# Optimization experiments

Measured on AMD Instinct MI355X. Metric: run time of the kernel, lower is better.

Reference implementation:

```python
import jax, jax.numpy as jnp
import numpy as np

N_NODES = 100000
N_EDGES = 1600000
IN_CH = 32
HID = 128
EDGE_DIM = 16
BN_EPS = 1e-5


def setup_inputs() -> dict:
    key = jax.random.key(0)
    ks = jax.random.split(key, 32)
    f32 = jnp.float32

    def w(k, shape, scale):
        return jax.random.normal(k, shape, dtype=f32) * scale

    inp = {
        'x': w(ks[0], (N_NODES, IN_CH), 1.0),
        'edge_index': jax.random.randint(ks[1], (2, N_EDGES), 0, N_NODES, dtype=jnp.int32),
        'edge_attr': w(ks[2], (N_EDGES, EDGE_DIM), 1.0),
        # layer 0: in=32 -> out=128
        'l0_We': w(ks[3], (EDGE_DIM, IN_CH), 0.1),
        'l0_be': jnp.zeros((IN_CH,), f32),
        'l0_W1': w(ks[4], (IN_CH, HID), 0.1),
        'l0_b1': jnp.zeros((HID,), f32),
        'l0_W2': w(ks[5], (HID, HID), 0.1),
        'l0_b2': jnp.zeros((HID,), f32),
        'l0_gamma': jnp.ones((HID,), f32),
        'l0_beta': jnp.zeros((HID,), f32),
        # layer 1: 128 -> 128
        'l1_We': w(ks[6], (EDGE_DIM, HID), 0.1),
        'l1_be': jnp.zeros((HID,), f32),
        'l1_W1': w(ks[7], (HID, HID), 0.1),
        'l1_b1': jnp.zeros((HID,), f32),
        'l1_W2': w(ks[8], (HID, HID), 0.1),
        'l1_b2': jnp.zeros((HID,), f32),
        'l1_gamma': jnp.ones((HID,), f32),
        'l1_beta': jnp.zeros((HID,), f32),
        # head MLP: hidden -> hidden -> 1
        'head_W1': w(ks[9], (HID, HID), 0.1),
        'head_b1': jnp.zeros((HID,), f32),
        'head_W2': w(ks[10], (HID, 1), 0.1),
        'head_b2': jnp.zeros((1,), f32),
    }
    return inp


def _gnblock(x, src, dst, e, We, be, W1, b1, W2, b2, gamma, beta):
    # GINE-style message passing: gather -> edge message -> scatter-sum
    msg = jax.nn.relu(x[src] + e @ We + be)              # [E, d_in]
    agg = jax.ops.segment_sum(msg, dst, num_segments=N_NODES)  # [N, d_in]
    h = x + agg                                          # GIN combine (eps=0)
    h = jax.nn.relu(h @ W1 + b1) @ W2 + b2               # 2-layer MLP
    # batch norm over the node dimension (use_norm=True)
    mu = jnp.mean(h, axis=0)
    var = jnp.var(h, axis=0)
    h = (h - mu) * jax.lax.rsqrt(var + BN_EPS) * gamma + beta
    return jax.nn.relu(h)


def reference(x, edge_index, edge_attr,
              l0_We, l0_be, l0_W1, l0_b1, l0_W2, l0_b2, l0_gamma, l0_beta,
              l1_We, l1_be, l1_W1, l1_b1, l1_W2, l1_b2, l1_gamma, l1_beta,
              head_W1, head_b1, head_W2, head_b2):
    src, dst = edge_index[0], edge_index[1]
    h = _gnblock(x, src, dst, edge_attr,
                 l0_We, l0_be, l0_W1, l0_b1, l0_W2, l0_b2, l0_gamma, l0_beta)
    h = _gnblock(h, src, dst, edge_attr,
                 l1_We, l1_be, l1_W1, l1_b1, l1_W2, l1_b2, l1_gamma, l1_beta)
    # MLPBlock head + sigmoid -> per-node selection probability [N, 1]
    out = jax.nn.relu(h @ head_W1 + head_b1) @ head_W2 + head_b2
    return jax.nn.sigmoid(out)
```

## Files before the change

kernel.cpp:

```cpp
#include <hip/hip_runtime.h>

#define NN 100000
#define NE 1600000
#define TMAX 193760
#define NRANGES 24220

typedef unsigned int uint32;
typedef unsigned long long ull;
typedef __attribute__((ext_vector_type(8))) short bf16x8;
typedef __attribute__((ext_vector_type(4))) float f32x4;

__device__ __forceinline__ unsigned short f2bf(float f) {
  unsigned int u = __float_as_uint(f);
  unsigned int r = (u + 0x7fffu + ((u >> 16) & 1u)) >> 16;
  return (unsigned short)r;
}
__device__ __forceinline__ float bf2f(unsigned short u) {
  return __uint_as_float(((unsigned int)u) << 16);
}
__device__ __forceinline__ unsigned int pack2(float a, float b) {
  return (unsigned int)f2bf(a) | ((unsigned int)f2bf(b) << 16);
}
__device__ __forceinline__ uint32 pack2ru(float a, float b) {
  const uint32 ua = __float_as_uint(a) + 0x8000u;
  const uint32 ub = __float_as_uint(b) + 0x8000u;
  return (ua >> 16) | (ub & 0xffff0000u);
}
__device__ __forceinline__ float row16_sum(float x) {
  x += __int_as_float(__builtin_amdgcn_mov_dpp(__float_as_int(x), 0x128, 0xf, 0xf, false));
  x += __int_as_float(__builtin_amdgcn_mov_dpp(__float_as_int(x), 0x124, 0xf, 0xf, false));
  x += __int_as_float(__builtin_amdgcn_mov_dpp(__float_as_int(x), 0x122, 0xf, 0xf, false));
  x += __int_as_float(__builtin_amdgcn_mov_dpp(__float_as_int(x), 0x121, 0xf, 0xf, false));
  return x;
}

__device__ __forceinline__ void wconv_body(const float* __restrict__ src,
    unsigned short* __restrict__ dst, int K, int N, int b)
{
  const int i = b * 256 + threadIdx.x;
  if (i < K * N) {
    const int n = i / K, k = i - n * K;
    dst[i] = f2bf(src[k * N + n]);
  }
}

__global__ __launch_bounds__(256) void conv_all(
    const float* __restrict__ l0W1, const float* __restrict__ l0W2,
    const float* __restrict__ l1W1, const float* __restrict__ l1W2,
    const float* __restrict__ hW1,  const float* __restrict__ l0We,
    const float* __restrict__ l1We, const float* __restrict__ x,
    unsigned short* __restrict__ W1t0, unsigned short* __restrict__ W2t0,
    unsigned short* __restrict__ W1t1, unsigned short* __restrict__ W2t1,
    unsigned short* __restrict__ hW1t, unsigned short* __restrict__ Wet0,
    unsigned short* __restrict__ Wet1, unsigned short* __restrict__ xb)
{
  int b = blockIdx.x;
  if (b < 16)  { wconv_body(l0W1, W1t0, 32, 128, b); return; }  b -= 16;
  if (b < 64)  { wconv_body(l0W2, W2t0, 128, 128, b); return; } b -= 64;
  if (b < 64)  { wconv_body(l1W1, W1t1, 128, 128, b); return; } b -= 64;
  if (b < 64)  { wconv_body(l1W2, W2t1, 128, 128, b); return; } b -= 64;
  if (b < 64)  { wconv_body(hW1,  hW1t, 128, 128, b); return; } b -= 64;
  if (b < 2)   { wconv_body(l0We, Wet0, 16, 32, b); return; }   b -= 2;
  if (b < 8)   { wconv_body(l1We, Wet1, 16, 128, b); return; }  b -= 8;
  const int i = b * 256 + threadIdx.x;
  if (i * 8 < NN * 32) {
    const float4 a = ((const float4*)x)[i * 2];
    const float4 d = ((const float4*)x)[i * 2 + 1];
    uint4 o;
    o.x = pack2(a.x, a.y); o.y = pack2(a.z, a.w);
    o.z = pack2(d.x, d.y); o.w = pack2(d.z, d.w);
    ((uint4*)xb)[i] = o;
  }
}

__global__ __launch_bounds__(256) void hist_kernel(
    const int* __restrict__ ei, uint32* __restrict__ deg)
{
  const int e = blockIdx.x * 256 + threadIdx.x;
  if (e < NE) atomicAdd(&deg[ei[NE + e]], 1u);
}

__global__ __launch_bounds__(256) void offsets2_kernel(
    const uint32* __restrict__ deg, uint32* __restrict__ toff,
    uint32* __restrict__ eoff, ull* __restrict__ counter)
{
  __shared__ ull s[256];
  __shared__ ull base;
  const int tid = threadIdx.x;
  const int n = blockIdx.x * 256 + tid;
  const uint32 d = (n < NN) ? deg[n] : 0u;
  const uint32 tc = (d + 15u) >> 4;
  const ull v = ((ull)tc << 32) | (ull)d;
  s[tid] = v;
  __syncthreads();
#pragma unroll
  for (int st = 1; st < 256; st <<= 1) {
    ull w = (tid >= st) ? s[tid - st] : 0ull;
    __syncthreads();
    s[tid] += w;
    __syncthreads();
  }
  if (tid == 255) base = atomicAdd(counter, s[255]);
  __syncthreads();
  if (n < NN) {
    const ull t = base + (s[tid] - v);
    toff[n] = (uint32)(t >> 32);
    eoff[n] = (uint32)t;
  }
}

__global__ __launch_bounds__(256) void snode_fill(
    const uint32* __restrict__ toff, const uint32* __restrict__ deg,
    int* __restrict__ snode)
{
  const int n = blockIdx.x * 256 + threadIdx.x;
  if (n < NN) {
    const uint32 t0 = toff[n];
    const uint32 tc = (deg[n] + 15u) >> 4;
    for (uint32 i = 0; i < tc; ++i) snode[t0 + i] = n;
  }
}

__global__ __launch_bounds__(256) void fill_kernel(
    const int* __restrict__ ei, const uint32* __restrict__ eoff,
    uint32* __restrict__ cnt, uint2* __restrict__ esrc2)
{
  const int e = blockIdx.x * 256 + threadIdx.x;
  if (e < NE) {
    const int dst = ei[NE + e];
    const uint32 pos = eoff[dst] + atomicAdd(&cnt[dst], 1u);
    esrc2[pos] = make_uint2((uint32)e, (uint32)ei[e]);
  }
}

template<int D, int NCT, bool GEA>
__global__ __launch_bounds__(256) void flat_agg5(
    const int* __restrict__ snode, const uint32* __restrict__ toff,
    const uint32* __restrict__ eoff, const uint32* __restrict__ deg,
    const uint2* __restrict__ esrc2, const float* __restrict__ ea,
    unsigned short* __restrict__ eabc,
    const unsigned short* __restrict__ hsrc,
    const unsigned short* __restrict__ Wet, const float* __restrict__ be,
    const ull* __restrict__ tot, float* __restrict__ agg)
{
  const int tid = threadIdx.x;
  const int wid = tid >> 6;
  const int lane = tid & 63;
  const int c = lane & 15;
  const int g = lane >> 4;
  constexpr bool HALF = (NCT * 16 != D);
  int range, ch0;
  if (HALF) { range = blockIdx.x * 2 + (wid >> 1); ch0 = (wid & 1) * (NCT * 16); }
  else      { range = blockIdx.x * 4 + wid;        ch0 = 0; }
  const int tile0 = range * 8;
  const uint32 ntile = (uint32)((*tot) >> 32);
  if ((uint32)tile0 >= ntile) return;

  bf16x8 wf[NCT];
#pragma unroll
  for (int ct = 0; ct < NCT; ++ct) {
    const int chA = ch0 + (c >> 2) * (NCT * 4) + ct * 4 + (c & 3);
    uint4 u = make_uint4(0u, 0u, 0u, 0u);
    if (g < 2) u = *(const uint4*)&Wet[chA * 16 + g * 8];
    else if (g == 2) u.x = (0xFE96u << 16) | (uint32)f2bf(be[chA]);
    union { uint4 u4; bf16x8 v; } cv; cv.u4 = u;
    wf[ct] = cv.v;
  }

  int sn8 = -1, pk8 = 0, p_ = 0;
  if (lane < 8) {
    sn8 = snode[tile0 + lane];
    if (sn8 >= 0) {
      const uint32 to = toff[sn8], dg = deg[sn8], eo = eoff[sn8];
      const int k = tile0 + lane - (int)to;
      p_ = (int)eo + k * 16;
      int rv = (int)dg - k * 16; if (rv > 16) rv = 16;
      const int fl = (k == 0 ? 1 : 0) |
                     ((k == (int)((dg + 15u) >> 4) - 1) ? 2 : 0);
      pk8 = (rv << 7) | (fl << 12);
    }
  }
  const int p0base = __shfl(p_, 0);
  if (lane < 8 && sn8 >= 0) pk8 |= (p_ - p0base);

  const uint2 q0 = esrc2[(size_t)p0base + lane];
  const uint2 q1 = esrc2[(size_t)p0base + 64 + lane];

  float acc[NCT][4];
#pragma unroll
  for (int ct = 0; ct < NCT; ++ct) {
    acc[ct][0] = 0.f; acc[ct][1] = 0.f; acc[ct][2] = 0.f; acc[ct][3] = 0.f;
  }
  int openNode = -1; bool openFull = false, openClosed = false;

  auto flushOpen = [&](bool storeOK) {
#pragma unroll
    for (int ct = 0; ct < NCT; ++ct)
#pragma unroll
      for (int j = 0; j < 4; ++j)
        acc[ct][j] = row16_sum(acc[ct][j]);
    float4 sv = make_float4(0.f, 0.f, 0.f, 0.f);
#pragma unroll
    for (int ct = 0; ct < NCT; ++ct)
      if (c == ct)
        sv = make_float4(acc[ct][0], acc[ct][1], acc[ct][2], acc[ct][3]);
    if (c < NCT) {
      float* p = &agg[(size_t)openNode * D + ch0 + g * (NCT * 4) + c * 4];
      if (storeOK) {
        *(float4*)p = sv;
      } else {
        atomicAdd(p + 0, sv.x); atomicAdd(p + 1, sv.y);
        atomicAdd(p + 2, sv.z); atomicAdd(p + 3, sv.w);
      }
    }
  };

  auto issue = [&](int t, float4& E0, float4& E1, uint4& afu,
                   uint4& h0, uint4& h1, int& n_, int& mt_) {
    n_ = __shfl(sn8, t);
    mt_ = __shfl(pk8, t);
    const int d0 = mt_ & 127;
    const int rem = (mt_ >> 7) & 31;
    const int idx = d0 + ((c < rem) ? c : 0);
    const int li = idx & 63;
    const uint32 sA = (uint32)__shfl((int)q0.y, li);
    const uint32 sB = (uint32)__shfl((int)q1.y, li);
    const int src = (int)((idx & 64) ? sB : sA);
    if constexpr (GEA) {
      const uint32 eA = (uint32)__shfl((int)q0.x, li);
      const uint32 eB = (uint32)__shfl((int)q1.x, li);
      const int e = (int)((idx & 64) ? eB : eA);
      if (g < 2) {
        E0 = *(const float4*)&ea[(size_t)e * 16 + g * 8];
        E1 = *(const float4*)&ea[(size_t)e * 16 + g * 8 + 4];
      }
    } else {
      if (g < 2) afu = *(const uint4*)&eabc[((size_t)p0base + idx) * 16 + g * 8];
    }
    h0 = *(const uint4*)&hsrc[(size_t)src * D + ch0 + g * (NCT * 4)];
    if constexpr (NCT == 4)
      h1 = *(const uint4*)&hsrc[(size_t)src * D + ch0 + g * (NCT * 4) + 8];
  };

  auto compute = [&](const float4 E0, const float4 E1, uint4 afu,
                     const uint4 h0, const uint4 h1, const int n, const int mt) {
    if (n < 0) return;
    const int rem = (mt >> 7) & 31;
    const int fl = mt >> 12;
    if (n != openNode) {
      if (openNode >= 0) {
        flushOpen(openFull);
#pragma unroll
        for (int ct = 0; ct < NCT; ++ct) {
          acc[ct][0] = 0.f; acc[ct][1] = 0.f;
          acc[ct][2] = 0.f; acc[ct][3] = 0.f;
        }
      }
      openNode = n; openFull = (fl & 1) != 0; openClosed = false;
    }
    if (fl & 2) openClosed = true;
    if constexpr (GEA) {
      afu.x = pack2ru(E0.x, E0.y); afu.y = pack2ru(E0.z, E0.w);
      afu.z = pack2ru(E1.x, E1.y); afu.w = pack2ru(E1.z, E1.w);
      if (g < 2) {
        const int d0 = mt & 127;
        const int idx = d0 + ((c < rem) ? c : 0);
        *(uint4*)&eabc[((size_t)p0base + idx) * 16 + g * 8] = afu;
      }
    }
    bf16x8 afv;
    {
      uint4 u = make_uint4(0u, 0u, 0u, 0u);
      if (g < 2) u = afu;
      else if (g == 2) u.x = (c < rem) ? 0x3f80u : 0x3f803f80u;
      union { uint4 u4; bf16x8 v; } cv; cv.u4 = u; afv = cv.v;
    }
#pragma unroll
    for (int ct = 0; ct < NCT; ++ct) {
      f32x4 pre = __builtin_amdgcn_mfma_f32_16x16x32_bf16(
          wf[ct], afv, (f32x4){0.f, 0.f, 0.f, 0.f}, 0, 0, 0);
      uint32 w0, w1;
      if constexpr (NCT == 4) {
        const uint4 hu = (ct < 2) ? h0 : h1;
        w0 = (ct & 1) ? hu.z : hu.x;
        w1 = (ct & 1) ? hu.w : hu.y;
      } else {
        w0 = (ct & 1) ? h0.z : h0.x;
        w1 = (ct & 1) ? h0.w : h0.y;
      }
      acc[ct][0] += fmaxf(pre[0] + bf2f((unsigned short)(w0 & 0xffffu)), 0.f);
      acc[ct][1] += fmaxf(pre[1] + bf2f((unsigned short)(w0 >> 16)), 0.f);
      acc[ct][2] += fmaxf(pre[2] + bf2f((unsigned short)(w1 & 0xffffu)), 0.f);
      acc[ct][3] += fmaxf(pre[3] + bf2f((unsigned short)(w1 >> 16)), 0.f);
    }
  };

  float4 eA0, eA1, eB0, eB1, eC0, eC1;
  uint4 aA = make_uint4(0,0,0,0), aB = make_uint4(0,0,0,0), aC = make_uint4(0,0,0,0);
  uint4 h0A = make_uint4(0,0,0,0), h1A = make_uint4(0,0,0,0);
  uint4 h0B = make_uint4(0,0,0,0), h1B = make_uint4(0,0,0,0);
  uint4 h0C = make_uint4(0,0,0,0), h1C = make_uint4(0,0,0,0);
  int nA = -1, mA = 0, nB = -1, mB = 0, nC = -1, mC = 0;

  issue(0, eA0, eA1, aA, h0A, h1A, nA, mA);
  issue(1, eB0, eB1, aB, h0B, h1B, nB, mB);
  issue(2, eC0, eC1, aC, h0C, h1C, nC, mC);
  compute(eA0, eA1, aA, h0A, h1A, nA, mA); issue(3, eA0, eA1, aA, h0A, h1A, nA, mA);
  compute(eB0, eB1, aB, h0B, h1B, nB, mB); issue(4, eB0, eB1, aB, h0B, h1B, nB, mB);
  compute(eC0, eC1, aC, h0C, h1C, nC, mC); issue(5, eC0, eC1, aC, h0C, h1C, nC, mC);
  compute(eA0, eA1, aA, h0A, h1A, nA, mA); issue(6, eA0, eA1, aA, h0A, h1A, nA, mA);
  compute(eB0, eB1, aB, h0B, h1B, nB, mB); issue(7, eB0, eB1, aB, h0B, h1B, nB, mB);
  compute(eC0, eC1, aC, h0C, h1C, nC, mC);
  compute(eA0, eA1, aA, h0A, h1A, nA, mA);
  compute(eB0, eB1, aB, h0B, h1B, nB, mB);
  if (openNode >= 0) flushOpen(openFull && openClosed);
}

template<int DIN, bool ABF16>
__global__ __launch_bounds__(256) void mlp_mfma(
    const float* __restrict__ a32, const unsigned short* __restrict__ abf,
    const float* __restrict__ agg,
    const unsigned short* __restrict__ W1t, const float* __restrict__ b1,
    const unsigned short* __restrict__ W2t, const float* __restrict__ b2,
    float* __restrict__ outp, float* __restrict__ stats, int nChunks)
{
  constexpr int P1 = (DIN == 128) ? 136 : 40;
  constexpr int KS1 = DIN / 32;
  __shared__ __align__(16) unsigned short hin[64 * P1];
  __shared__ __align__(16) unsigned short tls[64 * 136];
  const int tid = threadIdx.x;
  const int w = tid >> 6;
  const int lane = tid & 63;
  const int c = lane & 15, g = lane >> 4;
  const int cw = w * 32;

  bf16x8 B1[2][KS1], B2[2][4];
#pragma unroll
  for (int ct = 0; ct < 2; ++ct)
#pragma unroll
    for (int kk = 0; kk < KS1; ++kk)
      B1[ct][kk] = *(const bf16x8*)&W1t[(cw + ct * 16 + c) * DIN + kk * 32 + g * 8];
#pragma unroll
  for (int ct = 0; ct < 2; ++ct)
#pragma unroll
    for (int kk = 0; kk < 4; ++kk)
      B2[ct][kk] = *(const bf16x8*)&W2t[(cw + ct * 16 + c) * 128 + kk * 32 + g * 8];
  const float b1c0 = b1[cw + c], b1c1 = b1[cw + 16 + c];
  const float b2c0 = b2[cw + c], b2c1 = b2[cw + 16 + c];
  float lsum0 = 0.f, lsum1 = 0.f, lsq0 = 0.f, lsq1 = 0.f;

  for (int chunk = blockIdx.x; chunk < nChunks; chunk += gridDim.x) {
    const int base = chunk * 64;
    if constexpr (DIN == 128) {
#pragma unroll
      for (int p = 0; p < 4; ++p) {
        const int idx = tid + 256 * p;
        const int n = idx >> 4, k8 = idx & 15;
        const int node = base + n;
        uint4 ov = make_uint4(0u, 0u, 0u, 0u);
        if (node < NN) {
          const float4 g0 = *(const float4*)&agg[node * 128 + k8 * 8];
          const float4 g1 = *(const float4*)&agg[node * 128 + k8 * 8 + 4];
          const uint4 hv = *(const uint4*)&abf[node * 128 + k8 * 8];
          ov.x = pack2(bf2f((unsigned short)(hv.x & 0xffffu)) + g0.x,
                       bf2f((unsigned short)(hv.x >> 16)) + g0.y);
          ov.y = pack2(bf2f((unsigned short)(hv.y & 0xffffu)) + g0.z,
                       bf2f((unsigned short)(hv.y >> 16)) + g0.w);
          ov.z = pack2(bf2f((unsigned short)(hv.z & 0xffffu)) + g1.x,
                       bf2f((unsigned short)(hv.z >> 16)) + g1.y);
          ov.w = pack2(bf2f((unsigned short)(hv.w & 0xffffu)) + g1.z,
                       bf2f((unsigned short)(hv.w >> 16)) + g1.w);
        }
        *(uint4*)&hin[n * P1 + k8 * 8] = ov;
      }
    } else {
      const int n = tid >> 2, k8 = tid & 3;
      const int node = base + n;
      uint4 ov = make_uint4(0u, 0u, 0u, 0u);
      if (node < NN) {
        const float4 x0 = *(const float4*)&a32[node * 32 + k8 * 8];
        const float4 x1 = *(const float4*)&a32[node * 32 + k8 * 8 + 4];
        const float4 g0 = *(const float4*)&agg[node * 32 + k8 * 8];
        const float4 g1 = *(const float4*)&agg[node * 32 + k8 * 8 + 4];
        ov.x = pack2(x0.x + g0.x, x0.y + g0.y);
        ov.y = pack2(x0.z + g0.z, x0.w + g0.w);
        ov.z = pack2(x1.x + g1.x, x1.y + g1.y);
        ov.w = pack2(x1.z + g1.z, x1.w + g1.w);
      }
      *(uint4*)&hin[n * P1 + k8 * 8] = ov;
    }
    __syncthreads();
#pragma unroll
    for (int nt = 0; nt < 4; ++nt) {
      bf16x8 af[KS1];
#pragma unroll
      for (int kk = 0; kk < KS1; ++kk)
        af[kk] = *(const bf16x8*)&hin[(nt * 16 + c) * P1 + kk * 32 + g * 8];
      f32x4 acc0 = {0.f, 0.f, 0.f, 0.f}, acc1 = {0.f, 0.f, 0.f, 0.f};
#pragma unroll
      for (int kk = 0; kk < KS1; ++kk) {
        acc0 = __builtin_amdgcn_mfma_f32_16x16x32_bf16(af[kk], B1[0][kk], acc0, 0, 0, 0);
        acc1 = __builtin_amdgcn_mfma_f32_16x16x32_bf16(af[kk], B1[1][kk], acc1, 0, 0, 0);
      }
#pragma unroll
      for (int j = 0; j < 4; ++j) {
        const int row = nt * 16 + g * 4 + j;
        tls[row * 136 + cw + c]      = f2bf(fmaxf(acc0[j] + b1c0, 0.f));
        tls[row * 136 + cw + 16 + c] = f2bf(fmaxf(acc1[j] + b1c1, 0.f));
      }
    }
    __syncthreads();
#pragma unroll
    for (int nt = 0; nt < 4; ++nt) {
      bf16x8 af[4];
#pragma unroll
      for (int kk = 0; kk < 4; ++kk)
        af[kk] = *(const bf16x8*)&tls[(nt * 16 + c) * 136 + kk * 32 + g * 8];
      f32x4 acc0 = {0.f, 0.f, 0.f, 0.f}, acc1 = {0.f, 0.f, 0.f, 0.f};
#pragma unroll
      for (int kk = 0; kk < 4; ++kk) {
        acc0 = __builtin_amdgcn_mfma_f32_16x16x32_bf16(af[kk], B2[0][kk], acc0, 0, 0, 0);
        acc1 = __builtin_amdgcn_mfma_f32_16x16x32_bf16(af[kk], B2[1][kk], acc1, 0, 0, 0);
      }
#pragma unroll
      for (int j = 0; j < 4; ++j) {
        const int node = base + nt * 16 + g * 4 + j;
        if (node < NN) {
          const float v0 = acc0[j] + b2c0;
          const float v1 = acc1[j] + b2c1;
          outp[node * 128 + cw + c] = v0;
          outp[node * 128 + cw + 16 + c] = v1;
          lsum0 += v0; lsq0 += v0 * v0;
          lsum1 += v1; lsq1 += v1 * v1;
        }
      }
    }
  }
  lsum0 += __shfl_xor(lsum0, 16); lsum0 += __shfl_xor(lsum0, 32);
  lsum1 += __shfl_xor(lsum1, 16); lsum1 += __shfl_xor(lsum1, 32);
  lsq0  += __shfl_xor(lsq0, 16);  lsq0  += __shfl_xor(lsq0, 32);
  lsq1  += __shfl_xor(lsq1, 16);  lsq1  += __shfl_xor(lsq1, 32);
  if (lane < 16) {
    atomicAdd(&stats[cw + lane], lsum0);
    atomicAdd(&stats[cw + 16 + lane], lsum1);
    atomicAdd(&stats[128 + cw + lane], lsq0);
    atomicAdd(&stats[128 + cw + 16 + lane], lsq1);
  }
}

__global__ void bn_finalize(float* __restrict__ stats,
                            const float* __restrict__ gamma,
                            const float* __restrict__ beta)
{
  const int cc = threadIdx.x;
  const float inv_n = 1.0f / (float)NN;
  const float mu = stats[cc] * inv_n;
  float var = stats[128 + cc] * inv_n - mu * mu;
  var = fmaxf(var, 0.f);
  const float rs = rsqrtf(var + 1e-5f);
  const float sc = rs * gamma[cc];
  stats[256 + cc] = sc;
  stats[384 + cc] = beta[cc] - mu * sc;
}

__global__ __launch_bounds__(256) void bn_apply_bf16(
    const float* __restrict__ h, const float* __restrict__ stats,
    unsigned short* __restrict__ hb)
{
  const int idx = blockIdx.x * 256 + threadIdx.x;
  const int c4 = (idx & 31) * 4;
  const float4 sc = *(const float4*)&stats[256 + c4];
  const float4 sh = *(const float4*)&stats[384 + c4];
  const float4 v = ((const float4*)h)[idx];
  const float r0 = fmaxf(fmaf(v.x, sc.x, sh.x), 0.f);
  const float r1 = fmaxf(fmaf(v.y, sc.y, sh.y), 0.f);
  const float r2 = fmaxf(fmaf(v.z, sc.z, sh.z), 0.f);
  const float r3 = fmaxf(fmaf(v.w, sc.w, sh.w), 0.f);
  uint2 o;
  o.x = pack2(r0, r1);
  o.y = pack2(r2, r3);
  ((uint2*)hb)[idx] = o;
}

__global__ __launch_bounds__(256) void head_bn(
    const float* __restrict__ hpre, const float* __restrict__ stats,
    const unsigned short* __restrict__ W1t, const float* __restrict__ b1,
    const float* __restrict__ w2, const float* __restrict__ b2,
    float* __restrict__ out, int nChunks)
{
  __shared__ float pl[4][64];
  const int tid = threadIdx.x;
  const int w = tid >> 6;
  const int lane = tid & 63;
  const int c = lane & 15, g = lane >> 4;
  const int cw = w * 32;

  bf16x8 B1[2][4];
#pragma unroll
  for (int ct = 0; ct < 2; ++ct)
#pragma unroll
    for (int kk = 0; kk < 4; ++kk)
      B1[ct][kk] = *(const bf16x8*)&W1t[(cw + ct * 16 + c) * 128 + kk * 32 + g * 8];
  const float b1c0 = b1[cw + c], b1c1 = b1[cw + 16 + c];
  const float w2c0 = w2[cw + c], w2c1 = w2[cw + 16 + c];
  const float b2v = b2[0];
  float4 scq[4][2], shq[4][2];
#pragma unroll
  for (int kk = 0; kk < 4; ++kk) {
    const int cb = kk * 32 + g * 8;
    scq[kk][0] = *(const float4*)&stats[256 + cb];
    scq[kk][1] = *(const float4*)&stats[256 + cb + 4];
    shq[kk][0] = *(const float4*)&stats[384 + cb];
    shq[kk][1] = *(const float4*)&stats[384 + cb + 4];
  }

  for (int chunk = blockIdx.x; chunk < nChunks; chunk += gridDim.x) {
    const int base = chunk * 64;
    float p[4][4];
#pragma unroll
    for (int nt = 0; nt < 4; ++nt) {
      const int node = base + nt * 16 + c;
      bf16x8 af[4];
#pragma unroll
      for (int kk = 0; kk < 4; ++kk) {
        uint4 u = make_uint4(0u, 0u, 0u, 0u);
        if (node < NN) {
          const float4 v0 = *(const float4*)&hpre[(size_t)node * 128 + kk * 32 + g * 8];
          const float4 v1 = *(const float4*)&hpre[(size_t)node * 128 + kk * 32 + g * 8 + 4];
          const float4 s0 = scq[kk][0], s1 = scq[kk][1];
          const float4 h0 = shq[kk][0], h1 = shq[kk][1];
          u.x = pack2(fmaxf(fmaf(v0.x, s0.x, h0.x), 0.f),
                      fmaxf(fmaf(v0.y, s0.y, h0.y), 0.f));
          u.y = pack2(fmaxf(fmaf(v0.z, s0.z, h0.z), 0.f),
                      fmaxf(fmaf(v0.w, s0.w, h0.w), 0.f));
          u.z = pack2(fmaxf(fmaf(v1.x, s1.x, h1.x), 0.f),
                      fmaxf(fmaf(v1.y, s1.y, h1.y), 0.f));
          u.w = pack2(fmaxf(fmaf(v1.z, s1.z, h1.z), 0.f),
                      fmaxf(fmaf(v1.w, s1.w, h1.w), 0.f));
        }
        union { uint4 u4; bf16x8 v; } cv; cv.u4 = u;
        af[kk] = cv.v;
      }
      f32x4 acc0 = {0.f, 0.f, 0.f, 0.f}, acc1 = {0.f, 0.f, 0.f, 0.f};
#pragma unroll
      for (int kk = 0; kk < 4; ++kk) {
        acc0 = __builtin_amdgcn_mfma_f32_16x16x32_bf16(af[kk], B1[0][kk], acc0, 0, 0, 0);
        acc1 = __builtin_amdgcn_mfma_f32_16x16x32_bf16(af[kk], B1[1][kk], acc1, 0, 0, 0);
      }
#pragma unroll
      for (int j = 0; j < 4; ++j)
        p[nt][j] = fmaxf(acc0[j] + b1c0, 0.f) * w2c0 +
                   fmaxf(acc1[j] + b1c1, 0.f) * w2c1;
    }
#pragma unroll
    for (int dd = 1; dd <= 8; dd <<= 1)
#pragma unroll
      for (int nt = 0; nt < 4; ++nt)
#pragma unroll
        for (int j = 0; j < 4; ++j)
          p[nt][j] += __shfl_xor(p[nt][j], dd);
    if (c == 0) {
#pragma unroll
      for (int nt = 0; nt < 4; ++nt)
#pragma unroll
        for (int j = 0; j < 4; ++j)
          pl[w][nt * 16 + g * 4 + j] = p[nt][j];
    }
    __syncthreads();
    if (tid < 64) {
      const int node = base + tid;
      if (node < NN) {
        const float s = pl[0][tid] + pl[1][tid] + pl[2][tid] + pl[3][tid] + b2v;
        out[node] = 1.f / (1.f + expf(-s));
      }
    }
    __syncthreads();
  }
}

extern "C" void kernel_launch(void* const* d_in, const int* in_sizes, int n_in,
                              void* d_out, int out_size, void* d_ws, size_t ws_size,
                              hipStream_t stream)
{
  const float* x    = (const float*)d_in[0];
  const int*   ei   = (const int*)  d_in[1];
  const float* ea   = (const float*)d_in[2];
  const float* l0We = (const float*)d_in[3];
  const float* l0be = (const float*)d_in[4];
  const float* l0W1 = (const float*)d_in[5];
  const float* l0b1 = (const float*)d_in[6];
  const float* l0W2 = (const float*)d_in[7];
  const float* l0b2 = (const float*)d_in[8];
  const float* l0g  = (const float*)d_in[9];
  const float* l0bt = (const float*)d_in[10];
  const float* l1We = (const float*)d_in[11];
  const float* l1be = (const float*)d_in[12];
  const float* l1W1 = (const float*)d_in[13];
  const float* l1b1 = (const float*)d_in[14];
  const float* l1W2 = (const float*)d_in[15];
  const float* l1b2 = (const float*)d_in[16];
  const float* l1g  = (const float*)d_in[17];
  const float* l1bt = (const float*)d_in[18];
  const float* hW1  = (const float*)d_in[19];
  const float* hb1  = (const float*)d_in[20];
  const float* hW2  = (const float*)d_in[21];
  const float* hb2  = (const float*)d_in[22];
  float* out = (float*)d_out;

  float*  A    = (float*)d_ws;
  float*  AGG  = A + (size_t)NN * 128;
  unsigned short* hb = (unsigned short*)(AGG + (size_t)NN * 128);
  unsigned short* xb = hb + (size_t)NN * 128;
  uint32* deg     = (uint32*)(xb + (size_t)NN * 32);
  uint32* cnt     = deg + NN;
  uint32* toff    = cnt + NN;
  uint32* eoff    = toff + NN;
  ull*    counter = (ull*)(eoff + NN);
  int*    snode   = (int*)(counter + 2);
  uint2*  esrc2   = (uint2*)(snode + TMAX);
  float*  st0     = (float*)(esrc2 + NE + 128);
  float*  st1     = st0 + 512;
  unsigned short* W1t0 = (unsigned short*)(st1 + 512);
  unsigned short* W2t0 = W1t0 + 4096;
  unsigned short* W1t1 = W2t0 + 16384;
  unsigned short* W2t1 = W1t1 + 16384;
  unsigned short* hW1t = W2t1 + 16384;
  unsigned short* Wet0 = hW1t + 16384;
  unsigned short* Wet1 = Wet0 + 512;
  unsigned short* eabc = Wet1 + 2048;

  const size_t needed = (size_t)((char*)(eabc + (size_t)NE * 16) - (char*)d_ws);
  if (ws_size < needed) return;

  hipMemsetAsync(deg, 0, (size_t)2 * NN * 4, stream);
  hipMemsetAsync(counter, 0, 16, stream);
  hipMemsetAsync(snode, 0xFF, (size_t)TMAX * 4, stream);
  hipMemsetAsync(st0, 0, 4096, stream);
  hipMemsetAsync(AGG, 0, (size_t)NN * 32 * 4, stream);

  const int nChunks = (NN + 63) / 64;
  const int eBlocks = (NE + 255) / 256;

  conv_all<<<16 + 64 * 4 + 2 + 8 + 1563, 256, 0, stream>>>(
      l0W1, l0W2, l1W1, l1W2, hW1, l0We, l1We, x,
      W1t0, W2t0, W1t1, W2t1, hW1t, Wet0, Wet1, xb);

  hist_kernel<<<eBlocks, 256, 0, stream>>>(ei, deg);
  offsets2_kernel<<<(NN + 255) / 256, 256, 0, stream>>>(deg, toff, eoff, counter);
  snode_fill<<<(NN + 255) / 256, 256, 0, stream>>>(toff, deg, snode);
  fill_kernel<<<eBlocks, 256, 0, stream>>>(ei, eoff, cnt, esrc2);

  flat_agg5<32, 2, true><<<NRANGES / 4, 256, 0, stream>>>(
      snode, toff, eoff, deg, esrc2, ea, eabc, xb, Wet0, l0be, counter, AGG);
  mlp_mfma<32, false><<<782, 256, 0, stream>>>(x, (const unsigned short*)nullptr,
      AGG, W1t0, l0b1, W2t0, l0b2, A, st0, nChunks);
  hipMemsetAsync(AGG, 0, (size_t)NN * 128 * 4, stream);
  bn_finalize<<<1, 128, 0, stream>>>(st0, l0g, l0bt);
  bn_apply_bf16<<<(NN * 32) / 256, 256, 0, stream>>>(A, st0, hb);

  flat_agg5<128, 4, false><<<NRANGES / 2, 256, 0, stream>>>(
      snode, toff, eoff, deg, esrc2, ea, eabc, hb, Wet1, l1be, counter, AGG);
  mlp_mfma<128, true><<<782, 256, 0, stream>>>((const float*)nullptr, hb,
      AGG, W1t1, l1b1, W2t1, l1b2, A, st1, nChunks);
  bn_finalize<<<1, 128, 0, stream>>>(st1, l1g, l1bt);

  head_bn<<<782, 256, 0, stream>>>(A, st1, hW1t, hb1, hW2, hb2, out, nChunks);
}
```

Baseline: 554.0 us.

## Swap MFMA operand roles so channels map to lanes and edges to accumulator rows

After: 541.3 us. 2.3% less time.

```diff
diff --git a/kernel.cpp b/kernel.cpp
--- a/kernel.cpp
+++ b/kernel.cpp
@@ -25,13 +25,6 @@
   const uint32 ua = __float_as_uint(a) + 0x8000u;
   const uint32 ub = __float_as_uint(b) + 0x8000u;
   return (ua >> 16) | (ub & 0xffff0000u);
-}
-__device__ __forceinline__ float row16_sum(float x) {
-  x += __int_as_float(__builtin_amdgcn_mov_dpp(__float_as_int(x), 0x128, 0xf, 0xf, false));
-  x += __int_as_float(__builtin_amdgcn_mov_dpp(__float_as_int(x), 0x124, 0xf, 0xf, false));
-  x += __int_as_float(__builtin_amdgcn_mov_dpp(__float_as_int(x), 0x122, 0xf, 0xf, false));
-  x += __int_as_float(__builtin_amdgcn_mov_dpp(__float_as_int(x), 0x121, 0xf, 0xf, false));
-  return x;
 }
 
 __device__ __forceinline__ void wconv_body(const float* __restrict__ src,
@@ -133,8 +126,8 @@
   }
 }
 
-template<int D, int NCT, bool GEA>
-__global__ __launch_bounds__(256) void flat_agg5(
+template<int D, int NB, bool GEA>
+__global__ __launch_bounds__(256) void flat_agg8(
     const int* __restrict__ snode, const uint32* __restrict__ toff,
     const uint32* __restrict__ eoff, const uint32* __restrict__ deg,
     const uint2* __restrict__ esrc2, const float* __restrict__ ea,
@@ -148,21 +141,18 @@
   const int lane = tid & 63;
   const int c = lane & 15;
   const int g = lane >> 4;
-  constexpr bool HALF = (NCT * 16 != D);
-  int range, ch0;
-  if (HALF) { range = blockIdx.x * 2 + (wid >> 1); ch0 = (wid & 1) * (NCT * 16); }
-  else      { range = blockIdx.x * 4 + wid;        ch0 = 0; }
+  const int range = blockIdx.x * 4 + wid;
   const int tile0 = range * 8;
   const uint32 ntile = (uint32)((*tot) >> 32);
   if ((uint32)tile0 >= ntile) return;
 
-  bf16x8 wf[NCT];
-#pragma unroll
-  for (int ct = 0; ct < NCT; ++ct) {
-    const int chA = ch0 + (c >> 2) * (NCT * 4) + ct * 4 + (c & 3);
+  bf16x8 wf[NB];
+#pragma unroll
+  for (int ct = 0; ct < NB; ++ct) {
+    const int ch = c * NB + ct;
     uint4 u = make_uint4(0u, 0u, 0u, 0u);
-    if (g < 2) u = *(const uint4*)&Wet[chA * 16 + g * 8];
-    else if (g == 2) u.x = (0xFE96u << 16) | (uint32)f2bf(be[chA]);
+    if (g < 2) u = *(const uint4*)&Wet[ch * 16 + g * 8];
+    else if (g == 2) u.x = (0x3f80u << 16) | (uint32)f2bf(be[ch]);
     union { uint4 u4; bf16x8 v; } cv; cv.u4 = u;
     wf[ct] = cv.v;
   }
@@ -186,64 +176,69 @@
   const uint2 q0 = esrc2[(size_t)p0base + lane];
   const uint2 q1 = esrc2[(size_t)p0base + 64 + lane];
 
-  float acc[NCT][4];
-#pragma unroll
-  for (int ct = 0; ct < NCT; ++ct) {
-    acc[ct][0] = 0.f; acc[ct][1] = 0.f; acc[ct][2] = 0.f; acc[ct][3] = 0.f;
-  }
+  float acc[NB];
+#pragma unroll
+  for (int ct = 0; ct < NB; ++ct) acc[ct] = 0.f;
   int openNode = -1; bool openFull = false, openClosed = false;
 
   auto flushOpen = [&](bool storeOK) {
 #pragma unroll
-    for (int ct = 0; ct < NCT; ++ct)
-#pragma unroll
-      for (int j = 0; j < 4; ++j)
-        acc[ct][j] = row16_sum(acc[ct][j]);
-    float4 sv = make_float4(0.f, 0.f, 0.f, 0.f);
-#pragma unroll
-    for (int ct = 0; ct < NCT; ++ct)
-      if (c == ct)
-        sv = make_float4(acc[ct][0], acc[ct][1], acc[ct][2], acc[ct][3]);
-    if (c < NCT) {
-      float* p = &agg[(size_t)openNode * D + ch0 + g * (NCT * 4) + c * 4];
+    for (int ct = 0; ct < NB; ++ct) {
+      acc[ct] += __shfl_xor(acc[ct], 16);
+      acc[ct] += __shfl_xor(acc[ct], 32);
+    }
+    if (g == 0) {
+      float* p = &agg[(size_t)openNode * D + c * NB];
       if (storeOK) {
-        *(float4*)p = sv;
+        if constexpr (NB == 8) {
+          *(float4*)p = make_float4(acc[0], acc[1], acc[2], acc[3]);
+          *(float4*)(p + 4) = make_float4(acc[4], acc[5], acc[6], acc[7]);
+        } else {
+          *(float2*)p = make_float2(acc[0], acc[1]);
+        }
       } else {
-        atomicAdd(p + 0, sv.x); atomicAdd(p + 1, sv.y);
-        atomicAdd(p + 2, sv.z); atomicAdd(p + 3, sv.w);
+#pragma unroll
+        for (int ct = 0; ct < NB; ++ct) atomicAdd(p + ct, acc[ct]);
       }
     }
   };
 
   auto issue = [&](int t, float4& E0, float4& E1, uint4& afu,
-                   uint4& h0, uint4& h1, int& n_, int& mt_) {
+                   uint4* h, int& n_, int& mt_) {
     n_ = __shfl(sn8, t);
     mt_ = __shfl(pk8, t);
     const int d0 = mt_ & 127;
     const int rem = (mt_ >> 7) & 31;
-    const int idx = d0 + ((c < rem) ? c : 0);
-    const int li = idx & 63;
-    const uint32 sA = (uint32)__shfl((int)q0.y, li);
-    const uint32 sB = (uint32)__shfl((int)q1.y, li);
-    const int src = (int)((idx & 64) ? sB : sA);
+    const int idxA = d0 + ((c < rem) ? c : 0);
     if constexpr (GEA) {
-      const uint32 eA = (uint32)__shfl((int)q0.x, li);
-      const uint32 eB = (uint32)__shfl((int)q1.x, li);
-      const int e = (int)((idx & 64) ? eB : eA);
+      const int liA = idxA & 63;
+      const uint32 eA_ = (uint32)__shfl((int)q0.x, liA);
+      const uint32 eB_ = (uint32)__shfl((int)q1.x, liA);
+      const int e = (int)((idxA & 64) ? eB_ : eA_);
       if (g < 2) {
         E0 = *(const float4*)&ea[(size_t)e * 16 + g * 8];
         E1 = *(const float4*)&ea[(size_t)e * 16 + g * 8 + 4];
       }
     } else {
-      if (g < 2) afu = *(const uint4*)&eabc[((size_t)p0base + idx) * 16 + g * 8];
-    }
-    h0 = *(const uint4*)&hsrc[(size_t)src * D + ch0 + g * (NCT * 4)];
-    if constexpr (NCT == 4)
-      h1 = *(const uint4*)&hsrc[(size_t)src * D + ch0 + g * (NCT * 4) + 8];
+      if (g < 2) afu = *(const uint4*)&eabc[((size_t)p0base + idxA) * 16 + g * 8];
+    }
+#pragma unroll
+    for (int j = 0; j < 4; ++j) {
+      const int cj = 4 * g + j;
+      const int idxj = d0 + ((cj < rem) ? cj : 0);
+      const int lij = idxj & 63;
+      const uint32 s0_ = (uint32)__shfl((int)q0.y, lij);
+      const uint32 s1_ = (uint32)__shfl((int)q1.y, lij);
+      const int src = (int)((idxj & 64) ? s1_ : s0_);
+      if constexpr (D == 128)
+        h[j] = *(const uint4*)&hsrc[(size_t)src * 128 + c * 8];
+      else
+        h[j].x = *(const uint32*)&hsrc[(size_t)src * 32 + c * 2];
+    }
   };
 
   auto compute = [&](const float4 E0, const float4 E1, uint4 afu,
-                     const uint4 h0, const uint4 h1, const int n, const int mt) {
+                     const uint4* h, const int n, const int mt) {
     if (n < 0) return;
     const int rem = (mt >> 7) & 31;
     const int fl = mt >> 12;
@@ -251,10 +246,7 @@
       if (openNode >= 0) {
         flushOpen(openFull);
 #pragma unroll
-        for (int ct = 0; ct < NCT; ++ct) {
-          acc[ct][0] = 0.f; acc[ct][1] = 0.f;
-          acc[ct][2] = 0.f; acc[ct][3] = 0.f;
-        }
+        for (int ct = 0; ct < NB; ++ct) acc[ct] = 0.f;
       }
       openNode = n; openFull = (fl & 1) != 0; openClosed = false;
     }
@@ -264,55 +256,58 @@
       afu.z = pack2ru(E1.x, E1.y); afu.w = pack2ru(E1.z, E1.w);
       if (g < 2) {
         const int d0 = mt & 127;
-        const int idx = d0 + ((c < rem) ? c : 0);
-        *(uint4*)&eabc[((size_t)p0base + idx) * 16 + g * 8] = afu;
+        const int idxA = d0 + ((c < rem) ? c : 0);
+        *(uint4*)&eabc[((size_t)p0base + idxA) * 16 + g * 8] = afu;
       }
     }
     bf16x8 afv;
     {
       uint4 u = make_uint4(0u, 0u, 0u, 0u);
       if (g < 2) u = afu;
-      else if (g == 2) u.x = (c < rem) ? 0x3f80u : 0x3f803f80u;
+      else if (g == 2) u.x = 0x3f80u | (((c < rem) ? 0u : 0xFE96u) << 16);
       union { uint4 u4; bf16x8 v; } cv; cv.u4 = u; afv = cv.v;
     }
 #pragma unroll
-    for (int ct = 0; ct < NCT; ++ct) {
+    for (int ct = 0; ct < NB; ++ct) {
       f32x4 pre = __builtin_amdgcn_mfma_f32_16x16x32_bf16(
-          wf[ct], afv, (f32x4){0.f, 0.f, 0.f, 0.f}, 0, 0, 0);
-      uint32 w0, w1;
-      if constexpr (NCT == 4) {
-        const uint4 hu = (ct < 2) ? h0 : h1;
-        w0 = (ct & 1) ? hu.z : hu.x;
-        w1 = (ct & 1) ? hu.w : hu.y;
-      } else {
-        w0 = (ct & 1) ? h0.z : h0.x;
-        w1 = (ct & 1) ? h0.w : h0.y;
-      }
-      acc[ct][0] += fmaxf(pre[0] + bf2f((unsigned short)(w0 & 0xffffu)), 0.f);
-      acc[ct][1] += fmaxf(pre[1] + bf2f((unsigned short)(w0 >> 16)), 0.f);
-      acc[ct][2] += fmaxf(pre[2] + bf2f((unsigned short)(w1 & 0xffffu)), 0.f);
-      acc[ct][3] += fmaxf(pre[3] + bf2f((unsigned short)(w1 >> 16)), 0.f);
+          afv, wf[ct], (f32x4){0.f, 0.f, 0.f, 0.f}, 0, 0, 0);
+#pragma unroll
+      for (int j = 0; j < 4; ++j) {
+        uint32 wv;
+        if constexpr (D == 128) {
+          const int q = ct >> 1;
+          wv = (q == 0) ? h[j].x : (q == 1) ? h[j].y : (q == 2) ? h[j].z : h[j].w;
+        } else {
+          wv = h[j].x;
+        }
+        const unsigned short hu = (unsigned short)((ct & 1) ? (wv >> 16)
+                                                            : (wv & 0xffffu));
+        acc[ct] += fmaxf(pre[j] + bf2f(hu), 0.f);
+      }
     }
   };
 
   float4 eA0, eA1, eB0, eB1, eC0, eC1;
   uint4 aA = make_uint4(0,0,0,0), aB = make_uint4(0,0,0,0), aC = make_uint4(0,0,0,0);
-  uint4 h0A = make_uint4(0,0,0,0), h1A = make_uint4(0,0,0,0);
-  uint4 h0B = make_uint4(0,0,0,0), h1B = make_uint4(0,0,0,0);
-  uint4 h0C = make_uint4(0,0,0,0), h1C = make_uint4(0,0,0,0);
-  int nA = -1, mA = 0, nB = -1, mB = 0, nC = -1, mC = 0;
-
-  issue(0, eA0, eA1, aA, h0A, h1A, nA, mA);
-  issue(1, eB0, eB1, aB, h0B, h1B, nB, mB);
-  issue(2, eC0, eC1, aC, h0C, h1C, nC, mC);
-  compute(eA0, eA1, aA, h0A, h1A, nA, mA); issue(3, eA0, eA1, aA, h0A, h1A, nA, mA);
-  compute(eB0, eB1, aB, h0B, h1B, nB, mB); issue(4, eB0, eB1, aB, h0B, h1B, nB, mB);
-  compute(eC0, eC1, aC, h0C, h1C, nC, mC); issue(5, eC0, eC1, aC, h0C, h1C, nC, mC);
-  compute(eA0, eA1, aA, h0A, h1A, nA, mA); issue(6, eA0, eA1, aA, h0A, h1A, nA, mA);
-  compute(eB0, eB1, aB, h0B, h1B, nB, mB); issue(7, eB0, eB1, aB, h0B, h1B, nB, mB);
-  compute(eC0, eC1, aC, h0C, h1C, nC, mC);
-  compute(eA0, eA1, aA, h0A, h1A, nA, mA);
-  compute(eB0, eB1, aB, h0B, h1B, nB, mB);
+  uint4 hA[4], hB[4], hC[4];
+#pragma unroll
+  for (int j = 0; j < 4; ++j) {
+    hA[j] = make_uint4(0,0,0,0); hB[j] = make_uint4(0,0,0,0);
+    hC[j] = make_uint4(0,0,0,0);
+  }
+  int nA = -1, mA = 0, nB_ = -1, mB = 0, nC = -1, mC = 0;
+
+  issue(0, eA0, eA1, aA, hA, nA, mA);
+  issue(1, eB0, eB1, aB, hB, nB_, mB);
+  issue(2, eC0, eC1, aC, hC, nC, mC);
+  compute(eA0, eA1, aA, hA, nA, mA); issue(3, eA0, eA1, aA, hA, nA, mA);
+  compute(eB0, eB1, aB, hB, nB_, mB); issue(4, eB0, eB1, aB, hB, nB_, mB);
+  compute(eC0, eC1, aC, hC, nC, mC); issue(5, eC0, eC1, aC, hC, nC, mC);
+  compute(eA0, eA1, aA, hA, nA, mA); issue(6, eA0, eA1, aA, hA, nA, mA);
+  compute(eB0, eB1, aB, hB, nB_, mB); issue(7, eB0, eB1, aB, hB, nB_, mB);
+  compute(eC0, eC1, aC, hC, nC, mC);
+  compute(eA0, eA1, aA, hA, nA, mA);
+  compute(eB0, eB1, aB, hB, nB_, mB);
   if (openNode >= 0) flushOpen(openFull && openClosed);
 }
 
@@ -650,7 +645,7 @@
   snode_fill<<<(NN + 255) / 256, 256, 0, stream>>>(toff, deg, snode);
   fill_kernel<<<eBlocks, 256, 0, stream>>>(ei, eoff, cnt, esrc2);
 
-  flat_agg5<32, 2, true><<<NRANGES / 4, 256, 0, stream>>>(
+  flat_agg8<32, 2, true><<<NRANGES / 4, 256, 0, stream>>>(
       snode, toff, eoff, deg, esrc2, ea, eabc, xb, Wet0, l0be, counter, AGG);
   mlp_mfma<32, false><<<782, 256, 0, stream>>>(x, (const unsigned short*)nullptr,
       AGG, W1t0, l0b1, W2t0, l0b2, A, st0, nChunks);
@@ -658,7 +653,7 @@
   bn_finalize<<<1, 128, 0, stream>>>(st0, l0g, l0bt);
   bn_apply_bf16<<<(NN * 32) / 256, 256, 0, stream>>>(A, st0, hb);
 
-  flat_agg5<128, 4, false><<<NRANGES / 2, 256, 0, stream>>>(
+  flat_agg8<128, 8, false><<<NRANGES / 4, 256, 0, stream>>>(
       snode, toff, eoff, deg, esrc2, ea, eabc, hb, Wet1, l1be, counter, AGG);
   mlp_mfma<128, true><<<782, 256, 0, stream>>>((const float*)nullptr, hb,
       AGG, W1t1, l1b1, W2t1, l1b2, A, st1, nChunks);
```
